# Performance work log

Hardware: AMD Instinct MI355X
Metric: run time of the kernel (lower is better)

## Reference

```python
import jax, jax.numpy as jnp
import numpy as np

K = 1024  # codebook size
D = 256   # embedding dim


def setup_inputs() -> dict:
    key = jax.random.key(0)
    k1, k2 = jax.random.split(key)
    z_e_x = jax.random.normal(k1, (32, D, 32, 32), dtype=jnp.float32)  # NCHW
    # nn.Embedding weight initialized uniform(-1/K, 1/K)
    W = jax.random.uniform(k2, (K, D), dtype=jnp.float32, minval=-1.0 / K, maxval=1.0 / K)
    return {"z_e_x": z_e_x, "W": W}


def reference(z_e_x, W):
    # permute NCHW -> NHWC, flatten spatial, nearest-codebook lookup (vq)
    z = jnp.transpose(z_e_x, (0, 2, 3, 1))            # [B, H, Wd, D]
    B, H, Wd, Dd = z.shape
    flat = z.reshape(-1, Dd)                           # [N, D]
    # squared L2 distances: ||z||^2 - 2 z.W^T + ||W||^2
    z_sq = jnp.sum(flat * flat, axis=1, keepdims=True)         # [N, 1]
    w_sq = jnp.sum(W * W, axis=1)                               # [K]
    dists = z_sq - 2.0 * (flat @ W.T) + w_sq[None, :]           # [N, K]
    idx = jnp.argmin(dists, axis=1)                             # [N]
    latents = idx.reshape(B, H, Wd)                             # [B, H, Wd] int indices
    return latents
```

## Files before the change

### kernel.cpp

```cpp
#include <hip/hip_runtime.h>

#define NPOS 32768
#define DDIM 256
#define KCODES 1024

typedef __attribute__((ext_vector_type(8))) short bf16x8;
typedef __attribute__((ext_vector_type(4))) float f32x4;
typedef unsigned long long u64;

__device__ __forceinline__ float sqr_rn(float x) {
    float r = x * x;
    asm volatile("" : "+v"(r));
    return r;
}
__device__ __forceinline__ float add_rn(float a, float b) {
    float r = a + b;
    asm volatile("" : "+v"(r));
    return r;
}

__device__ __forceinline__ unsigned short f2bf(float x) {
    unsigned u = __float_as_uint(x);
    return (unsigned short)((u + 0x7fffu + ((u >> 16) & 1u)) >> 16);
}

__device__ __forceinline__ u64 packm(float s, int code) {
    unsigned b = __float_as_uint(s);
    unsigned mm = ((unsigned)((int)b >> 31)) | 0x80000000u;
    return ((u64)(b ^ mm) << 32) | (unsigned)code;
}

__global__ __launch_bounds__(256) void wprep(const float* __restrict__ W,
                                             float* __restrict__ wsq,
                                             unsigned short* __restrict__ wb16t) {
    const int t   = threadIdx.x;
    const int bid = blockIdx.x;
    const int row = bid * 16 + (t >> 4);
    const int j   = t & 15;
    const float* base = W + row * DDIM + (j & 7) + (j >> 3) * 128;
    float r = sqr_rn(base[0]);
#pragma unroll
    for (int i = 1; i < 16; ++i) r = add_rn(r, sqr_rn(base[i * 8]));
#pragma unroll
    for (int m = 1; m <= 8; m <<= 1) r = add_rn(r, __shfl_xor(r, m));
    if (j == 0) wsq[row] = r;
#pragma unroll
    for (int jj = 0; jj < 2; ++jj) {
        const int u  = t + jj * 256;
        const int n  = bid * 16 + (u >> 5);
        const int k8 = u & 31;
        const float4 f0 = *(const float4*)&W[n * DDIM + k8 * 8];
        const float4 f1 = *(const float4*)&W[n * DDIM + k8 * 8 + 4];
        bf16x8 o;
        o[0] = (short)f2bf(f0.x); o[1] = (short)f2bf(f0.y);
        o[2] = (short)f2bf(f0.z); o[3] = (short)f2bf(f0.w);
        o[4] = (short)f2bf(f1.x); o[5] = (short)f2bf(f1.y);
        o[6] = (short)f2bf(f1.z); o[7] = (short)f2bf(f1.w);
        const int kk = k8 >> 2, kq = k8 & 3;
        *(bf16x8*)&wb16t[(n >> 8) * 65536 + kk * 8192 + kq * 2048 + (n & 255) * 8] = o;
    }
}

#define ZS 260
__global__ __launch_bounds__(256)
void vq_fused(const float* __restrict__ z,
              const float* __restrict__ W,
              const float* __restrict__ wsq,
              const unsigned short* __restrict__ wb16t,
              int* __restrict__ out) {
    union Sm {
        unsigned short At[16384];
        float          Zs[32 * ZS];
    };
    __shared__ Sm  sm;
    __shared__ u64 redP[64 * 4];
    __shared__ u64 candL[64 * 8];

    const int t   = threadIdx.x;
    const int bid = blockIdx.x;
    const int img = bid >> 4;
    const int p0  = (bid & 15) * 64;

    {
        const float* zbase = z + img * (DDIM * 1024) + p0;
#pragma unroll
        for (int jj = 0; jj < 8; ++jj) {
            const int u_ = t + jj * 256;
            const int m  = u_ & 63;
            const int k8 = u_ >> 6;
            const float* src = zbase + k8 * 8192 + m;
            bf16x8 o;
#pragma unroll
            for (int e = 0; e < 8; ++e) o[e] = (short)f2bf(src[e * 1024]);
            *(bf16x8*)&sm.At[k8 * 512 + m * 8] = o;
        }
    }
    __syncthreads();

    const int w  = t >> 6;
    const int l  = t & 63;
    const int ln = l & 15;
    const int q  = l >> 4;
    const int mw = (w & 1) * 32;
    const int nh = w >> 1;
    const int nw = nh * 128;

    const char* aBase = (const char*)sm.At + q * 1024 + (mw + ln) * 16;
    const char* bBase = (const char*)wb16t + q * 4096 + (nw + ln) * 16;

#pragma unroll 1
    for (int nblk = 0; nblk < 4; ++nblk) {
        const int n0 = nblk * 256;
        float wq[8];
#pragma unroll
        for (int nf = 0; nf < 8; ++nf) wq[nf] = wsq[n0 + nw + nf * 16 + ln];

        f32x4 acc[2][8];
#pragma unroll
        for (int a = 0; a < 2; ++a)
#pragma unroll
            for (int b = 0; b < 8; ++b) acc[a][b] = (f32x4)(0.f);

        const char* bP = bBase + nblk * 131072;
        bf16x8 bA[8], bB[8];
#pragma unroll
        for (int nf = 0; nf < 8; ++nf) bA[nf] = *(const bf16x8*)(bP + nf * 256);

#pragma unroll 1
        for (int kk2 = 0; kk2 < 4; ++kk2) {
            const int kkE = kk2 * 2;
#pragma unroll
            for (int nf = 0; nf < 8; ++nf)
                bB[nf] = *(const bf16x8*)(bP + (kkE + 1) * 16384 + nf * 256);
            {
                bf16x8 afr[2];
#pragma unroll
                for (int mf = 0; mf < 2; ++mf)
                    afr[mf] = *(const bf16x8*)(aBase + kkE * 4096 + mf * 256);
#pragma unroll
                for (int nf = 0; nf < 8; ++nf)
#pragma unroll
                    for (int mf = 0; mf < 2; ++mf)
                        acc[mf][nf] = __builtin_amdgcn_mfma_f32_16x16x32_bf16(
                            afr[mf], bA[nf], acc[mf][nf], 0, 0, 0);
            }
            if (kk2 < 3) {
#pragma unroll
                for (int nf = 0; nf < 8; ++nf)
                    bA[nf] = *(const bf16x8*)(bP + (kkE + 2) * 16384 + nf * 256);
            }
            {
                bf16x8 afr[2];
#pragma unroll
                for (int mf = 0; mf < 2; ++mf)
                    afr[mf] = *(const bf16x8*)(aBase + (kkE + 1) * 4096 + mf * 256);
#pragma unroll
                for (int nf = 0; nf < 8; ++nf)
#pragma unroll
                    for (int mf = 0; mf < 2; ++mf)
                        acc[mf][nf] = __builtin_amdgcn_mfma_f32_16x16x32_bf16(
                            afr[mf], bB[nf], acc[mf][nf], 0, 0, 0);
            }
        }

#pragma unroll
        for (int mf = 0; mf < 2; ++mf) {
#pragma unroll
            for (int reg = 0; reg < 4; ++reg) {
                const int row = mw + mf * 16 + q * 4 + reg;
                float s0 = 1e30f, s1 = 1e30f;
                int   i0 = 0,     i1 = 0;
#pragma unroll
                for (int nf = 0; nf < 8; ++nf) {
                    const float s  = fmaf(-2.f, acc[mf][nf][reg], wq[nf]);
                    const int   cc = n0 + nw + nf * 16 + ln;
                    if (s < s0)      { s1 = s0; i1 = i0; s0 = s; i0 = cc; }
                    else if (s < s1) { s1 = s; i1 = cc; }
                }
                u64 c0 = packm(s0, i0), c1 = packm(s1, i1);
#pragma unroll
                for (int m = 1; m <= 8; m <<= 1) {
                    const u64 o0 = __shfl_xor(c0, m);
                    const u64 o1 = __shfl_xor(c1, m);
                    const u64 hi = (c0 < o0) ? o0 : c0;
                    c0 = (c0 < o0) ? c0 : o0;
                    const u64 lo = (c1 < o1) ? c1 : o1;
                    c1 = (hi < lo) ? hi : lo;
                }
                if (ln == 0) {
                    redP[row * 4 + nh * 2]     = c0;
                    redP[row * 4 + nh * 2 + 1] = c1;
                }
            }
        }
        __syncthreads();
        if (t < 64) {
            const u64 a = redP[t * 4],     b = redP[t * 4 + 1];
            const u64 c = redP[t * 4 + 2], d = redP[t * 4 + 3];
            const u64 m1 = (a < c) ? a : c;
            const u64 hi = (a < c) ? c : a;
            const u64 lo = (b < d) ? b : d;
            const u64 m2 = (hi < lo) ? hi : lo;
            candL[t * 8 + nblk * 2]     = m1;
            candL[t * 8 + nblk * 2 + 1] = m2;
        }
        __syncthreads();
    }

    const float* zimg = z + img * (DDIM * 1024) + p0;
#pragma unroll 1
    for (int ch = 0; ch < 2; ++ch) {
#pragma unroll
        for (int jj = 0; jj < 8; ++jj) {
            const int f4 = t + jj * 256;
            const int d = f4 >> 3, p4 = f4 & 7;
            const float4 v = *(const float4*)&zimg[d * 1024 + ch * 32 + p4 * 4];
            sm.Zs[(p4 * 4 + 0) * ZS + d] = v.x;
            sm.Zs[(p4 * 4 + 1) * ZS + d] = v.y;
            sm.Zs[(p4 * 4 + 2) * ZS + d] = v.z;
            sm.Zs[(p4 * 4 + 3) * ZS + d] = v.w;
        }
        __syncthreads();
        {
            const int pl = t >> 3, slot = t & 7;
            const float* zr = &sm.Zs[pl * ZS];

            float h0 = sqr_rn(zr[slot]);
            float h1 = sqr_rn(zr[128 + slot]);
#pragma unroll
            for (int i = 1; i < 16; ++i) {
                h0 = add_rn(h0, sqr_rn(zr[slot + 8 * i]));
                h1 = add_rn(h1, sqr_rn(zr[128 + slot + 8 * i]));
            }
#pragma unroll
            for (int m = 1; m <= 4; m <<= 1) {
                h0 = add_rn(h0, __shfl_xor(h0, m));
                h1 = add_rn(h1, __shfl_xor(h1, m));
            }
            const float zq = add_rn(h0, h1);

            const int code = (int)(unsigned)(candL[(ch * 32 + pl) * 8 + slot] & 0xffffffffULL);
            const float* wr = W + code * DDIM;
            float M = 0.f;
#pragma unroll 8
            for (int d4 = 0; d4 < 64; ++d4) {
                const float4 zv = *(const float4*)&zr[d4 * 4];
                const float4 wv = *(const float4*)&wr[d4 * 4];
                M = fmaf(zv.x, wv.x, M);
                M = fmaf(zv.y, wv.y, M);
                M = fmaf(zv.z, wv.z, M);
                M = fmaf(zv.w, wv.w, M);
            }
            const float s = add_rn(fmaf(-2.f, M, zq), wsq[code]);
            u64 v = ((u64)__float_as_uint(s) << 32) | (unsigned)code;
#pragma unroll
            for (int m = 1; m <= 4; m <<= 1) {
                const u64 o = __shfl_xor(v, m);
                if (o < v) v = o;
            }
            if (slot == 0) out[img * 1024 + p0 + ch * 32 + pl] = (int)(unsigned)(v & 0xffffffffULL);
        }
        __syncthreads();
    }
}

extern "C" void kernel_launch(void* const* d_in, const int* in_sizes, int n_in,
                              void* d_out, int out_size, void* d_ws, size_t ws_size,
                              hipStream_t stream) {
    const float* z = (const float*)d_in[0];
    const float* W = (const float*)d_in[1];
    int* out = (int*)d_out;

    char* ws = (char*)d_ws;
    float*          wsq   = (float*)ws;
    unsigned short* wb16t = (unsigned short*)(ws + 4096);

    wprep<<<KCODES / 16, 256, 0, stream>>>(W, wsq, wb16t);
    vq_fused<<<NPOS / 64, 256, 0, stream>>>(z, W, wsq, wb16t, out);
}
```

Before: 143.8 us.

## Stage codebook tiles through LDS with async global_load_lds double buffering

Doubles the block to 512 threads and 128 positions, so each block reuses every codebook tile across twice as many rows. Codebook bf16 tiles are now streamed into a double-buffered LDS region with direct global-to-LDS loads, one k-slice ahead, instead of being loaded per wave into registers from global memory. This cuts global/L2 traffic for W per position and overlaps the loads with MFMA work. In exchange it adds a block barrier every k-step, raises LDS use (fewer resident blocks per CU), and halves the grid to 256 blocks.

New measurement: 149.6 us. 4.0% more time.

```diff
diff --git a/kernel.cpp b/kernel.cpp
--- a/kernel.cpp
+++ b/kernel.cpp
@@ -28,6 +28,12 @@
     unsigned b = __float_as_uint(s);
     unsigned mm = ((unsigned)((int)b >> 31)) | 0x80000000u;
     return ((u64)(b ^ mm) << 32) | (unsigned)code;
+}
+
+__device__ __forceinline__ void gload_lds16(const void* g, void* l) {
+    __builtin_amdgcn_global_load_lds(
+        (const __attribute__((address_space(1))) void*)g,
+        (__attribute__((address_space(3))) void*)l, 16, 0, 0);
 }
 
 __global__ __launch_bounds__(256) void wprep(const float* __restrict__ W,
@@ -62,147 +68,144 @@
 }
 
 #define ZS 260
-__global__ __launch_bounds__(256)
+__global__ __launch_bounds__(512)
 void vq_fused(const float* __restrict__ z,
               const float* __restrict__ W,
               const float* __restrict__ wsq,
               const unsigned short* __restrict__ wb16t,
               int* __restrict__ out) {
     union Sm {
-        unsigned short At[16384];
-        float          Zs[32 * ZS];
+        unsigned short At[32768];
+        float          Zs[64 * ZS];
     };
-    __shared__ Sm  sm;
-    __shared__ u64 redP[64 * 4];
-    __shared__ u64 candL[64 * 8];
-
-    const int t   = threadIdx.x;
-    const int bid = blockIdx.x;
-    const int img = bid >> 4;
-    const int p0  = (bid & 15) * 64;
+    __shared__ Sm   sm;
+    __shared__ char Bb[2][16384];
+    __shared__ u64  redP[128 * 4];
+    __shared__ u64  candL[128 * 8];
+
+    const int t    = threadIdx.x;
+    const int lane = t & 63;
+    const int wid  = t >> 6;
+    const int bid  = blockIdx.x;
+    const int img  = bid >> 3;
+    const int p0   = (bid & 7) * 128;
 
     {
         const float* zbase = z + img * (DDIM * 1024) + p0;
 #pragma unroll
         for (int jj = 0; jj < 8; ++jj) {
-            const int u_ = t + jj * 256;
-            const int m  = u_ & 63;
-            const int k8 = u_ >> 6;
+            const int u_ = t + jj * 512;
+            const int m  = u_ & 127;
+            const int k8 = u_ >> 7;
             const float* src = zbase + k8 * 8192 + m;
             bf16x8 o;
 #pragma unroll
             for (int e = 0; e < 8; ++e) o[e] = (short)f2bf(src[e * 1024]);
-            *(bf16x8*)&sm.At[k8 * 512 + m * 8] = o;
-        }
+            *(bf16x8*)&sm.At[k8 * 1024 + m * 8] = o;
+        }
+    }
+
+    {
+        const char* gsrc = (const char*)wb16t + wid * 2048 + lane * 16;
+        char* ldst = &Bb[0][wid * 2048];
+        gload_lds16(gsrc, ldst);
+        gload_lds16(gsrc + 1024, ldst + 1024);
     }
     __syncthreads();
 
-    const int w  = t >> 6;
-    const int l  = t & 63;
-    const int ln = l & 15;
-    const int q  = l >> 4;
-    const int mw = (w & 1) * 32;
-    const int nh = w >> 1;
-    const int nw = nh * 128;
-
-    const char* aBase = (const char*)sm.At + q * 1024 + (mw + ln) * 16;
-    const char* bBase = (const char*)wb16t + q * 4096 + (nw + ln) * 16;
+    const int ln = lane & 15;
+    const int q  = lane >> 4;
+    const int mq = wid >> 1;
+    const int nh = wid & 1;
+
+    float wq[8];
+    f32x4 acc[2][8];
 
 #pragma unroll 1
-    for (int nblk = 0; nblk < 4; ++nblk) {
-        const int n0 = nblk * 256;
-        float wq[8];
-#pragma unroll
-        for (int nf = 0; nf < 8; ++nf) wq[nf] = wsq[n0 + nw + nf * 16 + ln];
-
-        f32x4 acc[2][8];
-#pragma unroll
-        for (int a = 0; a < 2; ++a)
-#pragma unroll
-            for (int b = 0; b < 8; ++b) acc[a][b] = (f32x4)(0.f);
-
-        const char* bP = bBase + nblk * 131072;
-        bf16x8 bA[8], bB[8];
-#pragma unroll
-        for (int nf = 0; nf < 8; ++nf) bA[nf] = *(const bf16x8*)(bP + nf * 256);
-
-#pragma unroll 1
-        for (int kk2 = 0; kk2 < 4; ++kk2) {
-            const int kkE = kk2 * 2;
+    for (int s = 0; s < 32; ++s) {
+        const int panel = s >> 3;
+        const int kk    = s & 7;
+        const int cur   = s & 1;
+
+        if (kk == 0) {
 #pragma unroll
             for (int nf = 0; nf < 8; ++nf)
-                bB[nf] = *(const bf16x8*)(bP + (kkE + 1) * 16384 + nf * 256);
-            {
-                bf16x8 afr[2];
-#pragma unroll
-                for (int mf = 0; mf < 2; ++mf)
-                    afr[mf] = *(const bf16x8*)(aBase + kkE * 4096 + mf * 256);
-#pragma unroll
-                for (int nf = 0; nf < 8; ++nf)
-#pragma unroll
-                    for (int mf = 0; mf < 2; ++mf)
-                        acc[mf][nf] = __builtin_amdgcn_mfma_f32_16x16x32_bf16(
-                            afr[mf], bA[nf], acc[mf][nf], 0, 0, 0);
-            }
-            if (kk2 < 3) {
-#pragma unroll
-                for (int nf = 0; nf < 8; ++nf)
-                    bA[nf] = *(const bf16x8*)(bP + (kkE + 2) * 16384 + nf * 256);
-            }
-            {
-                bf16x8 afr[2];
-#pragma unroll
-                for (int mf = 0; mf < 2; ++mf)
-                    afr[mf] = *(const bf16x8*)(aBase + (kkE + 1) * 4096 + mf * 256);
-#pragma unroll
-                for (int nf = 0; nf < 8; ++nf)
-#pragma unroll
-                    for (int mf = 0; mf < 2; ++mf)
-                        acc[mf][nf] = __builtin_amdgcn_mfma_f32_16x16x32_bf16(
-                            afr[mf], bB[nf], acc[mf][nf], 0, 0, 0);
-            }
-        }
-
-#pragma unroll
-        for (int mf = 0; mf < 2; ++mf) {
-#pragma unroll
-            for (int reg = 0; reg < 4; ++reg) {
-                const int row = mw + mf * 16 + q * 4 + reg;
-                float s0 = 1e30f, s1 = 1e30f;
-                int   i0 = 0,     i1 = 0;
-#pragma unroll
-                for (int nf = 0; nf < 8; ++nf) {
-                    const float s  = fmaf(-2.f, acc[mf][nf][reg], wq[nf]);
-                    const int   cc = n0 + nw + nf * 16 + ln;
-                    if (s < s0)      { s1 = s0; i1 = i0; s0 = s; i0 = cc; }
-                    else if (s < s1) { s1 = s; i1 = cc; }
+                wq[nf] = wsq[panel * 256 + nh * 128 + nf * 16 + ln];
+#pragma unroll
+            for (int a = 0; a < 2; ++a)
+#pragma unroll
+                for (int b = 0; b < 8; ++b) acc[a][b] = (f32x4)(0.f);
+        }
+
+        if (s < 31) {
+            const int s1  = s + 1;
+            const int off = (s1 >> 3) * 131072 + (s1 & 7) * 16384;
+            const char* gsrc = (const char*)wb16t + off + wid * 2048 + lane * 16;
+            char* ldst = &Bb[cur ^ 1][wid * 2048];
+            gload_lds16(gsrc, ldst);
+            gload_lds16(gsrc + 1024, ldst + 1024);
+        }
+
+        bf16x8 afr[2], bfr[8];
+        {
+            const char* ab = (const char*)sm.At + (kk * 4 + q) * 2048 + (mq * 32 + ln) * 16;
+            afr[0] = *(const bf16x8*)ab;
+            afr[1] = *(const bf16x8*)(ab + 256);
+            const char* bb = &Bb[cur][q * 4096 + (nh * 128 + ln) * 16];
+#pragma unroll
+            for (int nf = 0; nf < 8; ++nf)
+                bfr[nf] = *(const bf16x8*)(bb + nf * 256);
+        }
+#pragma unroll
+        for (int nf = 0; nf < 8; ++nf)
+#pragma unroll
+            for (int mf = 0; mf < 2; ++mf)
+                acc[mf][nf] = __builtin_amdgcn_mfma_f32_16x16x32_bf16(
+                    afr[mf], bfr[nf], acc[mf][nf], 0, 0, 0);
+
+        if (kk == 7) {
+            const int n0 = panel * 256;
+#pragma unroll
+            for (int mf = 0; mf < 2; ++mf) {
+#pragma unroll
+                for (int reg = 0; reg < 4; ++reg) {
+                    const int row = mq * 32 + mf * 16 + q * 4 + reg;
+                    float s0 = 1e30f, s1 = 1e30f;
+                    int   i0 = 0,     i1 = 0;
+#pragma unroll
+                    for (int nf = 0; nf < 8; ++nf) {
+                        const float sc = fmaf(-2.f, acc[mf][nf][reg], wq[nf]);
+                        const int   cc = n0 + nh * 128 + nf * 16 + ln;
+                        if (sc < s0)      { s1 = s0; i1 = i0; s0 = sc; i0 = cc; }
+                        else if (sc < s1) { s1 = sc; i1 = cc; }
+                    }
+                    u64 c0 = packm(s0, i0), c1 = packm(s1, i1);
+#pragma unroll
+                    for (int m = 1; m <= 8; m <<= 1) {
+                        const u64 o0 = __shfl_xor(c0, m);
+                        const u64 o1 = __shfl_xor(c1, m);
+                        const u64 hi = (c0 < o0) ? o0 : c0;
+                        c0 = (c0 < o0) ? c0 : o0;
+                        const u64 lo = (c1 < o1) ? c1 : o1;
+                        c1 = (hi < lo) ? hi : lo;
+                    }
+                    if (ln == 0) {
+                        redP[row * 4 + nh * 2]     = c0;
+                        redP[row * 4 + nh * 2 + 1] = c1;
+                    }
                 }
-                u64 c0 = packm(s0, i0), c1 = packm(s1, i1);
-#pragma unroll
-                for (int m = 1; m <= 8; m <<= 1) {
-                    const u64 o0 = __shfl_xor(c0, m);
-                    const u64 o1 = __shfl_xor(c1, m);
-                    const u64 hi = (c0 < o0) ? o0 : c0;
-                    c0 = (c0 < o0) ? c0 : o0;
-                    const u64 lo = (c1 < o1) ? c1 : o1;
-                    c1 = (hi < lo) ? hi : lo;
-                }
-                if (ln == 0) {
-                    redP[row * 4 + nh * 2]     = c0;
-                    redP[row * 4 + nh * 2 + 1] = c1;
-                }
-            }
-        }
-        __syncthreads();
-        if (t < 64) {
-            const u64 a = redP[t * 4],     b = redP[t * 4 + 1];
-            const u64 c = redP[t * 4 + 2], d = redP[t * 4 + 3];
-            const u64 m1 = (a < c) ? a : c;
-            const u64 hi = (a < c) ? c : a;
-            const u64 lo = (b < d) ? b : d;
-            const u64 m2 = (hi < lo) ? hi : lo;
-            candL[t * 8 + nblk * 2]     = m1;
-            candL[t * 8 + nblk * 2 + 1] = m2;
+            }
+            __syncthreads();
+            if (t < 128) {
+                const u64 a = redP[t * 4],     b = redP[t * 4 + 1];
+                const u64 c = redP[t * 4 + 2], d = redP[t * 4 + 3];
+                const u64 m1 = (a < c) ? a : c;
+                const u64 hi = (a < c) ? c : a;
+                const u64 lo = (b < d) ? b : d;
+                const u64 m2 = (hi < lo) ? hi : lo;
+                candL[t * 8 + panel * 2]     = m1;
+                candL[t * 8 + panel * 2 + 1] = m2;
+            }
         }
         __syncthreads();
     }
@@ -212,9 +215,9 @@
     for (int ch = 0; ch < 2; ++ch) {
 #pragma unroll
         for (int jj = 0; jj < 8; ++jj) {
-            const int f4 = t + jj * 256;
-            const int d = f4 >> 3, p4 = f4 & 7;
-            const float4 v = *(const float4*)&zimg[d * 1024 + ch * 32 + p4 * 4];
+            const int f4 = t + jj * 512;
+            const int d = f4 >> 4, p4 = f4 & 15;
+            const float4 v = *(const float4*)&zimg[d * 1024 + ch * 64 + p4 * 4];
             sm.Zs[(p4 * 4 + 0) * ZS + d] = v.x;
             sm.Zs[(p4 * 4 + 1) * ZS + d] = v.y;
             sm.Zs[(p4 * 4 + 2) * ZS + d] = v.z;
@@ -239,7 +242,7 @@
             }
             const float zq = add_rn(h0, h1);
 
-            const int code = (int)(unsigned)(candL[(ch * 32 + pl) * 8 + slot] & 0xffffffffULL);
+            const int code = (int)(unsigned)(candL[(ch * 64 + pl) * 8 + slot] & 0xffffffffULL);
             const float* wr = W + code * DDIM;
             float M = 0.f;
 #pragma unroll 8
@@ -251,14 +254,14 @@
                 M = fmaf(zv.z, wv.z, M);
                 M = fmaf(zv.w, wv.w, M);
             }
-            const float s = add_rn(fmaf(-2.f, M, zq), wsq[code]);
-            u64 v = ((u64)__float_as_uint(s) << 32) | (unsigned)code;
+            const float sc = add_rn(fmaf(-2.f, M, zq), wsq[code]);
+            u64 v = ((u64)__float_as_uint(sc) << 32) | (unsigned)code;
 #pragma unroll
             for (int m = 1; m <= 4; m <<= 1) {
                 const u64 o = __shfl_xor(v, m);
                 if (o < v) v = o;
             }
-            if (slot == 0) out[img * 1024 + p0 + ch * 32 + pl] = (int)(unsigned)(v & 0xffffffffULL);
+            if (slot == 0) out[img * 1024 + p0 + ch * 64 + pl] = (int)(unsigned)(v & 0xffffffffULL);
         }
         __syncthreads();
     }
@@ -276,5 +279,5 @@
     unsigned short* wb16t = (unsigned short*)(ws + 4096);
 
     wprep<<<KCODES / 16, 256, 0, stream>>>(W, wsq, wb16t);
-    vq_fused<<<NPOS / 64, 256, 0, stream>>>(z, W, wsq, wb16t, out);
-}
+    vq_fused<<<NPOS / 128, 512, 0, stream>>>(z, W, wsq, wb16t, out);
+}
```
